# Kernel optimization log

Measured on AMD Instinct MI355X. Metric: run time of the kernel, lower is better.

## Reference

```python
import jax, jax.numpy as jnp
from jax import lax
import numpy as np

B, T, F, H = 64, 512, 256, 512


def _gru_scan(data_tbf, Wi, bi, Wh, bhn):
    """Run a flax-style GRUCell over time. data_tbf: (T, B, F) -> (T, B, H)."""
    def step(h, x):
        xg = x @ Wi + bi              # (B, 3H): ir | iz | in
        hg = h @ Wh                   # (B, 3H): hr | hz | hn (hn bias added below)
        xr, xz, xn = jnp.split(xg, 3, axis=-1)
        hr, hz, hn = jnp.split(hg, 3, axis=-1)
        r = jax.nn.sigmoid(xr + hr)
        z = jax.nn.sigmoid(xz + hz)
        n = jnp.tanh(xn + r * (hn + bhn))
        new_h = (1.0 - z) * n + z * h
        return new_h, new_h

    h0 = jnp.zeros((data_tbf.shape[1], Wh.shape[0]), data_tbf.dtype)
    _, ys = lax.scan(step, h0, data_tbf)
    return ys


def setup_inputs() -> dict:
    key = jax.random.key(0)
    ks = jax.random.split(key, 5)
    s_i = 1.0 / np.sqrt(F)
    s_h = 1.0 / np.sqrt(H)
    return {
        "data": jax.random.normal(ks[0], (B, T, F), jnp.float32),
        "Wi_f": jax.random.normal(ks[1], (F, 3 * H), jnp.float32) * s_i,
        "bi_f": jnp.zeros((3 * H,), jnp.float32),
        "Wh_f": jax.random.normal(ks[2], (H, 3 * H), jnp.float32) * s_h,
        "bhn_f": jnp.zeros((H,), jnp.float32),
        "Wi_b": jax.random.normal(ks[3], (F, 3 * H), jnp.float32) * s_i,
        "bi_b": jnp.zeros((3 * H,), jnp.float32),
        "Wh_b": jax.random.normal(ks[4], (H, 3 * H), jnp.float32) * s_h,
        "bhn_b": jnp.zeros((H,), jnp.float32),
    }


def reference(data, Wi_f, bi_f, Wh_f, bhn_f, Wi_b, bi_b, Wh_b, bhn_b):
    # Forward direction: scan over time (axis 1 of data)
    fwd = _gru_scan(jnp.swapaxes(data, 0, 1), Wi_f, bi_f, Wh_f, bhn_f)
    fwd = jnp.swapaxes(fwd, 0, 1)                      # (B, T, H)
    # 'Backward' direction: source flips axis 0 (batch), faithfully reproduced.
    rev = jnp.flip(data, axis=0)
    bwd = _gru_scan(jnp.swapaxes(rev, 0, 1), Wi_b, bi_b, Wh_b, bhn_b)
    bwd = jnp.swapaxes(bwd, 0, 1)                      # (B, T, H)
    bwd = jnp.flip(bwd, axis=0)
    return jnp.concatenate([fwd, bwd], axis=-1)        # (B, T, 2H)
```

## Files before the change

kernel.cpp:

```cpp
#include <hip/hip_runtime.h>
#include <hip/hip_bf16.h>


#define TT 512
#define FF 256
#define HH 512
#define G3 1536
#define NSLICE 32
#define NWG 256
#define NTHR 64

typedef __attribute__((ext_vector_type(8))) short short8;
typedef __attribute__((ext_vector_type(4))) float f32x4;

__device__ __forceinline__ unsigned short f2bf(float f) {
  union { float f; unsigned u; } x; x.f = f;
  return (unsigned short)((x.u + 0x7fffu + ((x.u >> 16) & 1u)) >> 16);
}

__device__ __forceinline__ unsigned pk2(float a, float b) {
  union { __hip_bfloat162 h; unsigned u; } x;
  x.h = __float22bfloat162_rn(make_float2(a, b));
  return x.u;
}

__device__ __forceinline__ float sigm(float x) {
  return __builtin_amdgcn_rcpf(1.f + __expf(-x));
}

#define MFMA(a, b, c) __builtin_amdgcn_mfma_f32_16x16x32_bf16((a), (b), (c), 0, 0, 0)

__global__ __launch_bounds__(NTHR, 1) void gru_fused(
    const float* __restrict__ data,
    const float* __restrict__ Wi_f, const float* __restrict__ bi_f,
    const float* __restrict__ Wh_f, const float* __restrict__ bhn_f,
    const float* __restrict__ Wi_b, const float* __restrict__ bi_b,
    const float* __restrict__ Wh_b, const float* __restrict__ bhn_b,
    float* __restrict__ out,
    unsigned long long* __restrict__ hbuf,
    int* __restrict__ flags)
{
  const int wg   = blockIdx.x;
  const int unit = wg & 7;
  const int s    = wg >> 3;
  const int dir  = unit >> 2;
  const int bg   = unit & 3;
  const int lane = threadIdx.x;
  const int l15  = lane & 15;
  const int lg   = lane >> 4;

  const float* Wi  = dir ? Wi_b  : Wi_f;
  const float* Wh  = dir ? Wh_b  : Wh_f;
  const float* bi  = dir ? bi_b  : bi_f;
  const float* bhn = dir ? bhn_b : bhn_f;

  const int colT = s * 16 + l15;

  short8 whf[3][16];
#pragma unroll
  for (int g = 0; g < 3; ++g)
#pragma unroll
    for (int ks = 0; ks < 16; ++ks) {
      short8 v;
#pragma unroll
      for (int j = 0; j < 8; ++j)
        v[j] = (short)f2bf(Wh[(size_t)(ks * 32 + lg * 8 + j) * G3 + g * HH + colT]);
      whf[g][ks] = v;
    }
  short8 wif[3][8];
#pragma unroll
  for (int g = 0; g < 3; ++g)
#pragma unroll
    for (int ks = 0; ks < 8; ++ks) {
      short8 v;
#pragma unroll
      for (int j = 0; j < 8; ++j)
        v[j] = (short)f2bf(Wi[(size_t)(ks * 32 + lg * 8 + j) * G3 + g * HH + colT]);
      wif[g][ks] = v;
    }
  const float biR = bi[colT], biZ = bi[HH + colT], biN = bi[2 * HH + colT];
  const float bhnc = bhn[colT];

  int* myflags = flags + unit * TT;
  const float* xbase = data + (size_t)(bg * 16 + l15) * TT * FF;

  __shared__ __align__(16) unsigned short tile[16][16];

  float hp[4] = {0.f, 0.f, 0.f, 0.f};

  for (int t = 0; t < TT; ++t) {
    const int ib = t & 1;

    f32x4 accR = {0.f, 0.f, 0.f, 0.f};
    f32x4 accZ = {0.f, 0.f, 0.f, 0.f};
    f32x4 xN   = {0.f, 0.f, 0.f, 0.f};
    {
      const float* xr = xbase + (size_t)t * FF;
#pragma unroll
      for (int ks = 0; ks < 8; ++ks) {
        float4 x0 = *(const float4*)(xr + ks * 32 + lg * 8);
        float4 x1 = *(const float4*)(xr + ks * 32 + lg * 8 + 4);
        union { short8 s; unsigned u[4]; } a;
        a.u[0] = pk2(x0.x, x0.y); a.u[1] = pk2(x0.z, x0.w);
        a.u[2] = pk2(x1.x, x1.y); a.u[3] = pk2(x1.z, x1.w);
        accR = MFMA(a.s, wif[0][ks], accR);
        accZ = MFMA(a.s, wif[1][ks], accZ);
        xN   = MFMA(a.s, wif[2][ks], xN);
      }
    }

    if (t > 0) {
      while (__hip_atomic_load(&myflags[t - 1], __ATOMIC_RELAXED, __HIP_MEMORY_SCOPE_AGENT) < NSLICE)
        __builtin_amdgcn_s_sleep(1);
      __builtin_amdgcn_fence(__ATOMIC_ACQUIRE, "agent");
    }

    const unsigned long long* hin = hbuf + (size_t)(unit * 2 + ib) * 2048;
    unsigned long long q[32];
#pragma unroll
    for (int ks = 0; ks < 16; ++ks) {
      const int bidx = l15 * 128 + ks * 8 + lg * 2;
      q[2 * ks]     = __hip_atomic_load(&hin[bidx],     __ATOMIC_RELAXED, __HIP_MEMORY_SCOPE_AGENT);
      q[2 * ks + 1] = __hip_atomic_load(&hin[bidx + 1], __ATOMIC_RELAXED, __HIP_MEMORY_SCOPE_AGENT);
    }

    f32x4 hN = {0.f, 0.f, 0.f, 0.f};
#pragma unroll
    for (int ks = 0; ks < 16; ++ks) {
      union { short8 s; unsigned long long q[2]; } a;
      a.q[0] = q[2 * ks]; a.q[1] = q[2 * ks + 1];
      accR = MFMA(a.s, whf[0][ks], accR);
      accZ = MFMA(a.s, whf[1][ks], accZ);
      hN   = MFMA(a.s, whf[2][ks], hN);
    }

    float hv[4];
#pragma unroll
    for (int j = 0; j < 4; ++j) {
      float r = sigm(accR[j] + biR);
      float z = sigm(accZ[j] + biZ);
      float e = __expf(2.f * (xN[j] + biN + r * (hN[j] + bhnc)));
      float n = 1.f - 2.f * __builtin_amdgcn_rcpf(e + 1.f);
      hv[j] = (1.f - z) * n + z * hp[j];
      hp[j] = hv[j];
    }

#pragma unroll
    for (int j = 0; j < 4; ++j) tile[lg * 4 + j][l15] = f2bf(hv[j]);
    unsigned long long pv = *(const unsigned long long*)&tile[l15][lg * 4];
    unsigned long long* hout = hbuf + (size_t)(unit * 2 + (ib ^ 1)) * 2048;
    __hip_atomic_store(&hout[l15 * 128 + s * 4 + lg], pv,
                       __ATOMIC_RELAXED, __HIP_MEMORY_SCOPE_AGENT);
    asm volatile("s_waitcnt vmcnt(0)" ::: "memory");
    if (lane == 0)
      __hip_atomic_fetch_add(&myflags[t], 1, __ATOMIC_RELAXED, __HIP_MEMORY_SCOPE_AGENT);

#pragma unroll
    for (int j = 0; j < 4; ++j)
      out[((size_t)(bg * 16 + lg * 4 + j) * TT + t) * 1024 + (size_t)dir * HH + colT] = hv[j];
  }
}

extern "C" void kernel_launch(void* const* d_in, const int* in_sizes, int n_in,
                              void* d_out, int out_size, void* d_ws, size_t ws_size,
                              hipStream_t stream) {
  const float* data  = (const float*)d_in[0];
  const float* Wi_f  = (const float*)d_in[1];
  const float* bi_f  = (const float*)d_in[2];
  const float* Wh_f  = (const float*)d_in[3];
  const float* bhn_f = (const float*)d_in[4];
  const float* Wi_b  = (const float*)d_in[5];
  const float* bi_b  = (const float*)d_in[6];
  const float* Wh_b  = (const float*)d_in[7];
  const float* bhn_b = (const float*)d_in[8];
  float* out = (float*)d_out;

  unsigned long long* hbuf = (unsigned long long*)d_ws;
  int* flags = (int*)((char*)d_ws + 262144);
  hipMemsetAsync(d_ws, 0, 262144 + 16384, stream);

  gru_fused<<<NWG, NTHR, 0, stream>>>(data, Wi_f, bi_f, Wh_f, bhn_f,
                                      Wi_b, bi_b, Wh_b, bhn_b, out, hbuf, flags);
}
```

Before: 4.609 ms.

## Use per-slice progress flags and transposed MFMA to drop LDS transpose

Replaces the per-timestep shared counter (32 atomic increments, one poller spinning with sleep) with per-slice progress words that each workgroup stores, polled in parallel by lanes with a wave-wide all-check and no sleep. Swaps MFMA operand order so each lane holds four consecutive hidden columns for one batch row, which removes the LDS tile transpose before publishing h and lets the output be written as float4. Bias loads become per-lane vectors to match the new layout. The acquire fence is replaced by a compiler barrier only, which may weaken memory ordering on the hidden-state reads.

```diff
diff --git a/kernel.cpp b/kernel.cpp
--- a/kernel.cpp
+++ b/kernel.cpp
@@ -55,6 +55,7 @@
   const float* bhn = dir ? bhn_b : bhn_f;
 
   const int colT = s * 16 + l15;
+  const int colBase = s * 16 + lg * 4;
 
   short8 whf[3][16];
 #pragma unroll
@@ -78,13 +79,17 @@
         v[j] = (short)f2bf(Wi[(size_t)(ks * 32 + lg * 8 + j) * G3 + g * HH + colT]);
       wif[g][ks] = v;
     }
-  const float biR = bi[colT], biZ = bi[HH + colT], biN = bi[2 * HH + colT];
-  const float bhnc = bhn[colT];
+  float biR[4], biZ[4], biN[4], bhc[4];
+#pragma unroll
+  for (int j = 0; j < 4; ++j) {
+    biR[j] = bi[colBase + j];
+    biZ[j] = bi[HH + colBase + j];
+    biN[j] = bi[2 * HH + colBase + j];
+    bhc[j] = bhn[colBase + j];
+  }
 
-  int* myflags = flags + unit * TT;
+  int* myflags = flags + unit * 32;
   const float* xbase = data + (size_t)(bg * 16 + l15) * TT * FF;
-
-  __shared__ __align__(16) unsigned short tile[16][16];
 
   float hp[4] = {0.f, 0.f, 0.f, 0.f};
 
@@ -103,16 +108,19 @@
         union { short8 s; unsigned u[4]; } a;
         a.u[0] = pk2(x0.x, x0.y); a.u[1] = pk2(x0.z, x0.w);
         a.u[2] = pk2(x1.x, x1.y); a.u[3] = pk2(x1.z, x1.w);
-        accR = MFMA(a.s, wif[0][ks], accR);
-        accZ = MFMA(a.s, wif[1][ks], accZ);
-        xN   = MFMA(a.s, wif[2][ks], xN);
+        accR = MFMA(wif[0][ks], a.s, accR);
+        accZ = MFMA(wif[1][ks], a.s, accZ);
+        xN   = MFMA(wif[2][ks], a.s, xN);
       }
     }
 
     if (t > 0) {
-      while (__hip_atomic_load(&myflags[t - 1], __ATOMIC_RELAXED, __HIP_MEMORY_SCOPE_AGENT) < NSLICE)
-        __builtin_amdgcn_s_sleep(1);
-      __builtin_amdgcn_fence(__ATOMIC_ACQUIRE, "agent");
+      const int fidx = lane & 31;
+      while (true) {
+        int fl = __hip_atomic_load(&myflags[fidx], __ATOMIC_RELAXED, __HIP_MEMORY_SCOPE_AGENT);
+        if (__all(fl >= t)) break;
+      }
+      asm volatile("" ::: "memory");
     }
 
     const unsigned long long* hin = hbuf + (size_t)(unit * 2 + ib) * 2048;
@@ -129,35 +137,33 @@
     for (int ks = 0; ks < 16; ++ks) {
       union { short8 s; unsigned long long q[2]; } a;
       a.q[0] = q[2 * ks]; a.q[1] = q[2 * ks + 1];
-      accR = MFMA(a.s, whf[0][ks], accR);
-      accZ = MFMA(a.s, whf[1][ks], accZ);
-      hN   = MFMA(a.s, whf[2][ks], hN);
+      accR = MFMA(whf[0][ks], a.s, accR);
+      accZ = MFMA(whf[1][ks], a.s, accZ);
+      hN   = MFMA(whf[2][ks], a.s, hN);
     }
 
     float hv[4];
 #pragma unroll
     for (int j = 0; j < 4; ++j) {
-      float r = sigm(accR[j] + biR);
-      float z = sigm(accZ[j] + biZ);
-      float e = __expf(2.f * (xN[j] + biN + r * (hN[j] + bhnc)));
+      float r = sigm(accR[j] + biR[j]);
+      float z = sigm(accZ[j] + biZ[j]);
+      float e = __expf(2.f * (xN[j] + biN[j] + r * (hN[j] + bhc[j])));
       float n = 1.f - 2.f * __builtin_amdgcn_rcpf(e + 1.f);
       hv[j] = (1.f - z) * n + z * hp[j];
       hp[j] = hv[j];
     }
 
-#pragma unroll
-    for (int j = 0; j < 4; ++j) tile[lg * 4 + j][l15] = f2bf(hv[j]);
-    unsigned long long pv = *(const unsigned long long*)&tile[l15][lg * 4];
+    unsigned long long pv = (unsigned long long)pk2(hv[0], hv[1])
+                          | ((unsigned long long)pk2(hv[2], hv[3]) << 32);
     unsigned long long* hout = hbuf + (size_t)(unit * 2 + (ib ^ 1)) * 2048;
     __hip_atomic_store(&hout[l15 * 128 + s * 4 + lg], pv,
                        __ATOMIC_RELAXED, __HIP_MEMORY_SCOPE_AGENT);
     asm volatile("s_waitcnt vmcnt(0)" ::: "memory");
     if (lane == 0)
-      __hip_atomic_fetch_add(&myflags[t], 1, __ATOMIC_RELAXED, __HIP_MEMORY_SCOPE_AGENT);
+      __hip_atomic_store(&myflags[s], t + 1, __ATOMIC_RELAXED, __HIP_MEMORY_SCOPE_AGENT);
 
-#pragma unroll
-    for (int j = 0; j < 4; ++j)
-      out[((size_t)(bg * 16 + lg * 4 + j) * TT + t) * 1024 + (size_t)dir * HH + colT] = hv[j];
+    *(float4*)(out + ((size_t)(bg * 16 + l15) * TT + t) * 1024 + (size_t)dir * HH + colBase)
+        = make_float4(hv[0], hv[1], hv[2], hv[3]);
   }
 }
 
@@ -177,7 +183,7 @@
 
   unsigned long long* hbuf = (unsigned long long*)d_ws;
   int* flags = (int*)((char*)d_ws + 262144);
-  hipMemsetAsync(d_ws, 0, 262144 + 16384, stream);
+  hipMemsetAsync(d_ws, 0, 262144 + 4096, stream);
 
   gru_fused<<<NWG, NTHR, 0, stream>>>(data, Wi_f, bi_f, Wh_f, bhn_f,
                                       Wi_b, bi_b, Wh_b, bhn_b, out, hbuf, flags);
```

After: 3.732 ms. 19.0% less time.
